# Optimization experiments

Measured on AMD Instinct MI355X. Metric: run time of the kernel, lower is better.

The kernel has to match this reference:

```python
import jax, jax.numpy as jnp
import numpy as np

DIM, HEADS, FEAT = 512, 8, 128
HEAD_DIM = DIM // HEADS
B, N = 1, 2048
EPS = 1e-8


def setup_inputs() -> dict:
    key = jax.random.key(0)
    k1, k2, k3, k4 = jax.random.split(key, 4)
    x = jax.random.normal(k1, (B, N, DIM), dtype=jnp.float32)
    proj_matrix = jax.random.normal(k2, (HEADS, HEAD_DIM, FEAT), dtype=jnp.float32) / np.sqrt(HEAD_DIM)
    W_qkv = jax.random.normal(k3, (DIM, 3 * DIM), dtype=jnp.float32) * np.sqrt(2.0 / DIM)
    W_out = jax.random.normal(k4, (DIM, DIM), dtype=jnp.float32) * np.sqrt(2.0 / DIM)
    b_out = jnp.zeros((DIM,), dtype=jnp.float32)
    return {"x": x, "proj_matrix": proj_matrix, "W_qkv": W_qkv, "W_out": W_out, "b_out": b_out}


def _feature_map(t):
    return jax.nn.elu(t) + 1.0


def reference(x, proj_matrix, W_qkv, W_out, b_out):
    b, n, d = x.shape
    h, hd = HEADS, HEAD_DIM
    qkv = x @ W_qkv                      # (b,n,3d)
    q, k, v = jnp.split(qkv, 3, axis=-1)
    # (b,n,d) -> (b,h,n,hd)
    def to_heads(t):
        return t.reshape(b, n, h, hd).transpose(0, 2, 1, 3)
    q, k, v = to_heads(q), to_heads(k), to_heads(v)
    q_proj = _feature_map(jnp.einsum('bhnd,hdf->bhnf', q, proj_matrix))
    k_proj = _feature_map(jnp.einsum('bhnd,hdf->bhnf', k, proj_matrix))
    # causal linear attention via prefix sums (matches torch cumsum branch)
    k_cum = jnp.cumsum(k_proj, axis=2)                                   # (b,h,n,f)
    kv_cum = jnp.cumsum(k_proj[..., None] * v[..., None, :], axis=2)     # (b,h,n,f,hd)
    attn = jnp.einsum('bhnf,bhnfd->bhnd', q_proj, kv_cum)
    denom = jnp.einsum('bhnf,bhnf->bhn', q_proj, k_cum)[..., None]
    attn = attn / (denom + EPS)
    attn = attn.transpose(0, 2, 1, 3).reshape(b, n, d)
    return attn @ W_out + b_out
```

## Files before the change

### kernel.cpp

```cpp
#include <hip/hip_runtime.h>
#include <math.h>

#define NTOK 2048
#define DMODEL 512
#define NH 8
#define HD 64
#define NF 128
#define QKV_LD 1536
#define CHUNK 64
#define NCHUNK 32
#define EPS_C 1e-8f

typedef __bf16 bf16x8 __attribute__((ext_vector_type(8)));
typedef float f32x4 __attribute__((ext_vector_type(4)));

__device__ inline unsigned short f2bf(float f) {
  union { float f; unsigned u; } v; v.f = f;
  unsigned r = v.u + 0x7FFF + ((v.u >> 16) & 1);
  return (unsigned short)(r >> 16);
}


__global__ __launch_bounds__(256) void pack_all(
    const float* __restrict__ x, const float* __restrict__ W_qkv,
    const float* __restrict__ W_out, const float* __restrict__ proj,
    unsigned short* __restrict__ xpk, unsigned short* __restrict__ wqkvpk,
    unsigned short* __restrict__ woutpk, unsigned short* __restrict__ projpk,
    unsigned short* __restrict__ vT_pk)
{
  const int tid = blockIdx.x * 256 + threadIdx.x;
  const int job = blockIdx.y;
  unsigned short o[8];
  if (job == 0) {
    if (tid >= 131072) return;
    const int lane = tid & 63, blk = tid >> 6;
    const int bk = blk & 15, bm = blk >> 4;
    const int m = bm * 16 + (lane & 15), k = bk * 32 + (lane >> 4) * 8;
    const float4 v0 = *(const float4*)&x[(size_t)m * 512 + k];
    const float4 v1 = *(const float4*)&x[(size_t)m * 512 + k + 4];
    o[0] = f2bf(v0.x); o[1] = f2bf(v0.y); o[2] = f2bf(v0.z); o[3] = f2bf(v0.w);
    o[4] = f2bf(v1.x); o[5] = f2bf(v1.y); o[6] = f2bf(v1.z); o[7] = f2bf(v1.w);
    *(ushort4*)&xpk[(size_t)tid * 8]     = *(ushort4*)&o[0];
    *(ushort4*)&xpk[(size_t)tid * 8 + 4] = *(ushort4*)&o[4];
  } else if (job == 1) {
    if (tid >= 98304) return;
    const int lane = tid & 63, blk = tid >> 6;
    const int bk = blk & 15, bn = blk >> 4;
    const int n = bn * 16 + (lane & 15), k = bk * 32 + (lane >> 4) * 8;
#pragma unroll
    for (int e = 0; e < 8; ++e) o[e] = f2bf(W_qkv[(size_t)(k + e) * QKV_LD + n]);
    *(ushort4*)&wqkvpk[(size_t)tid * 8]     = *(ushort4*)&o[0];
    *(ushort4*)&wqkvpk[(size_t)tid * 8 + 4] = *(ushort4*)&o[4];
  } else if (job == 2) {
    if (tid >= 32768) return;
    const int lane = tid & 63, blk = tid >> 6;
    const int bk = blk & 15, bn = blk >> 4;
    const int n = bn * 16 + (lane & 15), k = bk * 32 + (lane >> 4) * 8;
#pragma unroll
    for (int e = 0; e < 8; ++e) o[e] = f2bf(W_out[(size_t)(k + e) * DMODEL + n]);
    *(ushort4*)&woutpk[(size_t)tid * 8]     = *(ushort4*)&o[0];
    *(ushort4*)&woutpk[(size_t)tid * 8 + 4] = *(ushort4*)&o[4];
  } else if (job == 3) {
    if (tid >= 8192) return;
    const int lane = tid & 63, blk = (tid >> 6) & 15, h = tid >> 10;
    const int bk = blk & 1, bn = blk >> 1;
    const int n = bn * 16 + (lane & 15), k = bk * 32 + (lane >> 4) * 8;
#pragma unroll
    for (int e = 0; e < 8; ++e) o[e] = f2bf(proj[(size_t)h * HD * NF + (size_t)(k + e) * NF + n]);
    *(ushort4*)&projpk[(size_t)tid * 8]     = *(ushort4*)&o[0];
    *(ushort4*)&projpk[(size_t)tid * 8 + 4] = *(ushort4*)&o[4];
  } else {
    if (tid >= 32768) return;
    const int hc = tid >> 7, kt = (tid >> 6) & 1, lane = tid & 63;
    const unsigned short val = ((lane & 15) == 0) ? (unsigned short)0x3F80 : (unsigned short)0;
    const size_t u = (size_t)hc * 640 + (4 * 2 + kt) * 64 + lane;
#pragma unroll
    for (int e = 0; e < 8; ++e) o[e] = val;
    *(ushort4*)&vT_pk[u * 8]     = *(ushort4*)&o[0];
    *(ushort4*)&vT_pk[u * 8 + 4] = *(ushort4*)&o[4];
  }
}

template<bool BIAS, int EMIT>
__global__ __launch_bounds__(256) void gemm_pk(
    const unsigned short* __restrict__ Apk, const unsigned short* __restrict__ Bpk,
    const float* __restrict__ bias, float* __restrict__ Cf,
    unsigned short* __restrict__ qkv_pk, unsigned short* __restrict__ vT_pk,
    int K, int ldc)
{
  const int lane = threadIdx.x & 63, w = threadIdx.x >> 6;
  const int wr = w >> 1, wc = w & 1;
  const int m0 = blockIdx.y * 64 + wr * 32;
  const int n0 = blockIdx.x * 64 + wc * 32;
  const int ks = K >> 5;
  const unsigned short* a0 = Apk + ((size_t)(m0 >> 4) * ks * 64 + lane) * 8;
  const unsigned short* a1 = a0 + (size_t)ks * 512;
  const unsigned short* b0 = Bpk + ((size_t)(n0 >> 4) * ks * 64 + lane) * 8;
  const unsigned short* b1 = b0 + (size_t)ks * 512;
  f32x4 acc00 = {0.f, 0.f, 0.f, 0.f}, acc01 = acc00, acc10 = acc00, acc11 = acc00;
#pragma unroll 4
  for (int s = 0; s < ks; ++s) {
    const bf16x8 af0 = *(const bf16x8*)(a0 + (size_t)s * 512);
    const bf16x8 af1 = *(const bf16x8*)(a1 + (size_t)s * 512);
    const bf16x8 bv0 = *(const bf16x8*)(b0 + (size_t)s * 512);
    const bf16x8 bv1 = *(const bf16x8*)(b1 + (size_t)s * 512);
    acc00 = __builtin_amdgcn_mfma_f32_16x16x32_bf16(af0, bv0, acc00, 0, 0, 0);
    acc01 = __builtin_amdgcn_mfma_f32_16x16x32_bf16(af0, bv1, acc01, 0, 0, 0);
    acc10 = __builtin_amdgcn_mfma_f32_16x16x32_bf16(af1, bv0, acc10, 0, 0, 0);
    acc11 = __builtin_amdgcn_mfma_f32_16x16x32_bf16(af1, bv1, acc11, 0, 0, 0);
  }
  const int r16 = lane & 15, kg = lane >> 4;
#pragma unroll
  for (int mb = 0; mb < 2; ++mb) {
#pragma unroll
    for (int nb = 0; nb < 2; ++nb) {
      const f32x4 a = mb == 0 ? (nb == 0 ? acc00 : acc01) : (nb == 0 ? acc10 : acc11);
      const int col = n0 + nb * 16 + r16;
      if (EMIT == 1) {
        if (col < 1024) {
          const int src = col >> 9, h = (col >> 6) & 7;
          const size_t base = (size_t)(src * 8 + h) * 16384 +
              ((size_t)((m0 >> 4) + mb) * 2 + wc) * 64 +
              ((nb * 2 + (r16 >> 3)) & 3) * 16;
          const int elem = r16 & 7;
#pragma unroll
          for (int r = 0; r < 4; ++r)
            qkv_pk[(base + kg * 4 + r) * 8 + elem] = f2bf(a[r]);
        } else {
          const int h = (col >> 6) - 16, c = blockIdx.y;
          const int vc = col & 63;
          const size_t u = (size_t)(h * 32 + c) * 640 +
              ((size_t)(vc >> 4) * 2 + wr) * 64 + (vc & 15) + (mb * 2 + (kg >> 1)) * 16;
          ushort4 rr;
          rr.x = f2bf(a[0]); rr.y = f2bf(a[1]); rr.z = f2bf(a[2]); rr.w = f2bf(a[3]);
          *(ushort4*)&vT_pk[u * 8 + (kg & 1) * 4] = rr;
        }
      } else {
        const float bv = BIAS ? bias[col] : 0.f;
#pragma unroll
        for (int r = 0; r < 4; ++r)
          Cf[(size_t)(m0 + mb * 16 + kg * 4 + r) * ldc + col] = a[r] + bv;
      }
    }
  }
}

__global__ __launch_bounds__(256) void proj_sums(
    const unsigned short* __restrict__ qkv_pk, const unsigned short* __restrict__ projpk,
    const unsigned short* __restrict__ vT_pk,
    unsigned short* __restrict__ q_pk, unsigned short* __restrict__ k_pk,
    float* __restrict__ kvsum)
{
  __shared__ unsigned short kT[8192];
  const int lane = threadIdx.x & 63, w = threadIdx.x >> 6;
  const int wr = w & 1, wc = w >> 1;
  const int c = blockIdx.x, src = blockIdx.y, h = blockIdx.z;
  const int r16 = lane & 15, kg = lane >> 4;
  const unsigned short* abase = qkv_pk + (size_t)(src * 8 + h) * 16384 * 8;
  const unsigned short* bbase = projpk + (size_t)h * 1024 * 8 + (size_t)lane * 8;
  f32x4 acc[2][4] = {};
#pragma unroll
  for (int s = 0; s < 2; ++s) {
#pragma unroll
    for (int mb = 0; mb < 2; ++mb) {
      const bf16x8 af = *(const bf16x8*)(abase +
          (((size_t)(c * 4 + wr * 2 + mb) * 2 + s) * 64 + lane) * 8);
#pragma unroll
      for (int nb = 0; nb < 4; ++nb) {
        const bf16x8 bv = *(const bf16x8*)(bbase + (size_t)((wc * 4 + nb) * 2 + s) * 512);
        acc[mb][nb] = __builtin_amdgcn_mfma_f32_16x16x32_bf16(af, bv, acc[mb][nb], 0, 0, 0);
      }
    }
  }
  unsigned short* dst = (src ? k_pk : q_pk) + (size_t)h * 32768 * 8;
#pragma unroll
  for (int mb = 0; mb < 2; ++mb) {
#pragma unroll
    for (int nb = 0; nb < 4; ++nb) {
      unsigned short vb[4];
#pragma unroll
      for (int r = 0; r < 4; ++r) {
        const float v = acc[mb][nb][r];
        vb[r] = f2bf(v > 0.f ? v + 1.f : expf(v));
      }
      const size_t base = ((size_t)(c * 4 + wr * 2 + mb) * 4 + wc * 2 + (nb >> 1)) * 64 +
                          ((nb & 1) * 2 + (r16 >> 3)) * 16;
      const int elem = r16 & 7;
#pragma unroll
      for (int r = 0; r < 4; ++r)
        dst[(base + kg * 4 + r) * 8 + elem] = vb[r];
      if (src == 1) {
        const size_t u = ((size_t)(wc * 4 + nb) * 2 + wr) * 64 + r16 + (mb * 2 + (kg >> 1)) * 16;
        *(ushort4*)&kT[u * 8 + (kg & 1) * 4] = *(ushort4*)&vb[0];
      }
    }
  }
  if (src == 1) {
    __syncthreads();
    const int wr2 = w >> 1, wc2 = w & 1;
    const int nnt = wc2 ? 2 : 3;
    const int ntb = wc2 ? 3 : 0;
    const unsigned short* vb_base = vT_pk + (size_t)(h * 32 + c) * 640 * 8;
    f32x4 acc2[4][3] = {};
#pragma unroll
    for (int ks = 0; ks < 2; ++ks) {
      bf16x8 bfr[3];
      for (int j = 0; j < 3; ++j)
        if (j < nnt)
          bfr[j] = *(const bf16x8*)(vb_base + (((size_t)(ntb + j) * 2 + ks) * 64 + lane) * 8);
#pragma unroll
      for (int amb = 0; amb < 4; ++amb) {
        const bf16x8 af = *(const bf16x8*)&kT[((((size_t)(wr2 * 4 + amb)) * 2 + ks) * 64 + lane) * 8];
        for (int j = 0; j < 3; ++j)
          if (j < nnt)
            acc2[amb][j] = __builtin_amdgcn_mfma_f32_16x16x32_bf16(af, bfr[j], acc2[amb][j], 0, 0, 0);
      }
    }
    float* outp = kvsum + (size_t)(h * 32 + c) * 128 * 80;
#pragma unroll
    for (int amb = 0; amb < 4; ++amb)
      for (int j = 0; j < 3; ++j)
        if (j < nnt) {
          const int colv = (ntb + j) * 16 + r16;
#pragma unroll
          for (int r = 0; r < 4; ++r)
            outp[(size_t)(wr2 * 64 + amb * 16 + kg * 4 + r) * 80 + colv] = acc2[amb][j][r];
        }
  }
}

__global__ __launch_bounds__(256) void chunk_scan(
    const float* __restrict__ kvsum, unsigned short* __restrict__ kvpre_pk)
{
  const int tid = blockIdx.x * 256 + threadIdx.x;
  if (tid >= 10240) return;
  const int h = tid / 1280, rem = tid % 1280;
  const int f8 = rem / 80, vc = rem % 80;
  float run[8] = {};
  const size_t u = ((size_t)(vc >> 4) * 4 + (f8 >> 2)) * 64 + (vc & 15) + (f8 & 3) * 16;
  for (int c = 0; c < NCHUNK; ++c) {
    unsigned short o[8];
#pragma unroll
    for (int e = 0; e < 8; ++e) o[e] = f2bf(run[e]);
    unsigned short* dst = kvpre_pk + ((size_t)(h * 32 + c) * 1280 + u) * 8;
    *(ushort4*)&dst[0] = *(ushort4*)&o[0];
    *(ushort4*)&dst[4] = *(ushort4*)&o[4];
    const float* srcp = kvsum + ((size_t)(h * 32 + c) * 128 + f8 * 8) * 80 + vc;
#pragma unroll
    for (int e = 0; e < 8; ++e) run[e] += srcp[(size_t)e * 80];
  }
}

__global__ __launch_bounds__(256) void chunk_attn(
    const unsigned short* __restrict__ q_pk, const unsigned short* __restrict__ k_pk,
    const unsigned short* __restrict__ kvpre_pk, const unsigned short* __restrict__ vT_pk,
    unsigned short* __restrict__ attn_pk)
{
  __shared__ unsigned short P[4096];
  __shared__ float den[64];
  const int lane = threadIdx.x & 63, w = threadIdx.x >> 6;
  const int wr = w >> 1, wc = w & 1;
  const int c = blockIdx.x, h = blockIdx.y;
  const int r16 = lane & 15, kg = lane >> 4;
  const unsigned short* qb = q_pk + (size_t)h * 32768 * 8;
  const unsigned short* kb = k_pk + (size_t)h * 32768 * 8;
  bf16x8 qa[2][4];
#pragma unroll
  for (int amb = 0; amb < 2; ++amb)
#pragma unroll
    for (int ks = 0; ks < 4; ++ks)
      qa[amb][ks] = *(const bf16x8*)(qb +
          (((size_t)(c * 4 + wr * 2 + amb) * 4 + ks) * 64 + lane) * 8);
  {
    f32x4 accS[2][2] = {};
#pragma unroll
    for (int ks = 0; ks < 4; ++ks) {
#pragma unroll
      for (int bnb = 0; bnb < 2; ++bnb) {
        const bf16x8 bf = *(const bf16x8*)(kb +
            (((size_t)(c * 4 + wc * 2 + bnb) * 4 + ks) * 64 + lane) * 8);
#pragma unroll
        for (int amb = 0; amb < 2; ++amb)
          accS[amb][bnb] = __builtin_amdgcn_mfma_f32_16x16x32_bf16(qa[amb][ks], bf, accS[amb][bnb], 0, 0, 0);
      }
    }
#pragma unroll
    for (int amb = 0; amb < 2; ++amb)
#pragma unroll
      for (int bnb = 0; bnb < 2; ++bnb) {
        const int ck = wc * 32 + bnb * 16 + r16;
        const size_t u = ((size_t)(wr * 2 + amb) * 2 + wc) * 64 + (bnb * 2 + (r16 >> 3)) * 16;
        const int elem = r16 & 7;
#pragma unroll
        for (int r = 0; r < 4; ++r) {
          const int rq = wr * 32 + amb * 16 + kg * 4 + r;
          P[(u + kg * 4 + r) * 8 + elem] = (ck <= rq) ? f2bf(accS[amb][bnb][r]) : (unsigned short)0;
        }
      }
  }
  __syncthreads();
  const int nnt = wc ? 2 : 3;
  const int ntb = wc ? 3 : 0;
  const unsigned short* kvp = kvpre_pk + (size_t)(h * 32 + c) * 1280 * 8;
  const unsigned short* vtb = vT_pk + (size_t)(h * 32 + c) * 640 * 8;
  f32x4 acc[2][3] = {};
#pragma unroll
  for (int ks = 0; ks < 4; ++ks) {
    bf16x8 bfr[3];
    for (int j = 0; j < 3; ++j)
      if (j < nnt)
        bfr[j] = *(const bf16x8*)(kvp + (((size_t)(ntb + j) * 4 + ks) * 64 + lane) * 8);
#pragma unroll
    for (int amb = 0; amb < 2; ++amb)
      for (int j = 0; j < 3; ++j)
        if (j < nnt)
          acc[amb][j] = __builtin_amdgcn_mfma_f32_16x16x32_bf16(qa[amb][ks], bfr[j], acc[amb][j], 0, 0, 0);
  }
#pragma unroll
  for (int ks = 0; ks < 2; ++ks) {
    bf16x8 bfr[3];
    for (int j = 0; j < 3; ++j)
      if (j < nnt)
        bfr[j] = *(const bf16x8*)(vtb + (((size_t)(ntb + j) * 2 + ks) * 64 + lane) * 8);
#pragma unroll
    for (int amb = 0; amb < 2; ++amb) {
      const bf16x8 pf = *(const bf16x8*)&P[((((size_t)(wr * 2 + amb)) * 2 + ks) * 64 + lane) * 8];
      for (int j = 0; j < 3; ++j)
        if (j < nnt)
          acc[amb][j] = __builtin_amdgcn_mfma_f32_16x16x32_bf16(pf, bfr[j], acc[amb][j], 0, 0, 0);
    }
  }
  if (wc == 1 && r16 == 0) {
#pragma unroll
    for (int amb = 0; amb < 2; ++amb)
#pragma unroll
      for (int r = 0; r < 4; ++r)
        den[wr * 32 + amb * 16 + kg * 4 + r] = acc[amb][1][r] + EPS_C;
  }
  __syncthreads();
#pragma unroll
  for (int amb = 0; amb < 2; ++amb) {
    for (int j = 0; j < 3; ++j) {
      const int nt = ntb + j;
      if (nt >= 4 || j >= nnt) continue;
      const int acol = h * 64 + nt * 16 + r16;
      const size_t base = ((size_t)(c * 4 + wr * 2 + amb) * 16 + (acol >> 5)) * 64 +
                          ((nt * 2 + (r16 >> 3)) & 3) * 16;
      const int elem = acol & 7;
#pragma unroll
      for (int r = 0; r < 4; ++r) {
        const float dinv = 1.0f / den[wr * 32 + amb * 16 + kg * 4 + r];
        attn_pk[(base + kg * 4 + r) * 8 + elem] = f2bf(acc[amb][j][r] * dinv);
      }
    }
  }
}

extern "C" void kernel_launch(void* const* d_in, const int* in_sizes, int n_in,
                              void* d_out, int out_size, void* d_ws, size_t ws_size,
                              hipStream_t stream) {
  const float* x     = (const float*)d_in[0];
  const float* proj  = (const float*)d_in[1];
  const float* W_qkv = (const float*)d_in[2];
  const float* W_out = (const float*)d_in[3];
  const float* b_out = (const float*)d_in[4];
  float* out = (float*)d_out;

  float* kvsum = (float*)d_ws;
  unsigned short* xpk     = (unsigned short*)(kvsum + 2621440);
  unsigned short* wqkvpk  = xpk + 1048576;
  unsigned short* woutpk  = wqkvpk + 786432;
  unsigned short* projpk  = woutpk + 262144;
  unsigned short* qkv_pk  = projpk + 65536;
  unsigned short* q_pk    = qkv_pk + 2097152;
  unsigned short* k_pk    = q_pk + 2097152;
  unsigned short* vT_pk   = k_pk + 2097152;
  unsigned short* kvpre_pk= vT_pk + 1310720;
  unsigned short* attn_pk = kvpre_pk + 2621440;

  pack_all<<<dim3(512, 5), 256, 0, stream>>>(x, W_qkv, W_out, proj,
                                             xpk, wqkvpk, woutpk, projpk, vT_pk);
  gemm_pk<false, 1><<<dim3(QKV_LD / 64, NTOK / 64), 256, 0, stream>>>(
      xpk, wqkvpk, nullptr, nullptr, qkv_pk, vT_pk, DMODEL, 0);
  proj_sums<<<dim3(NCHUNK, 2, NH), 256, 0, stream>>>(
      qkv_pk, projpk, vT_pk, q_pk, k_pk, kvsum);
  chunk_scan<<<dim3(40), 256, 0, stream>>>(kvsum, kvpre_pk);
  chunk_attn<<<dim3(NCHUNK, NH), 256, 0, stream>>>(
      q_pk, k_pk, kvpre_pk, vT_pk, attn_pk);
  gemm_pk<true, 0><<<dim3(DMODEL / 64, NTOK / 64), 256, 0, stream>>>(
      attn_pk, woutpk, b_out, out, nullptr, nullptr, DMODEL, DMODEL);
}
```

Measured before the change: 55.81 us.

## Fuse QKV GEMM with feature projection and merge chunk sums into scan

The QKV GEMM kernel now stages each 64x64 Q/K tile in shared memory and applies the per-head feature projection and ELU+1 in the same block, writing packed q/k and a transposed k layout directly. The separate proj_sums and chunk_scan kernels are replaced by one sums_scan kernel that computes each chunk's k^T v with MFMA and accumulates the running prefix in registers across chunks. This removes the intermediate qkv_pk and fp32 kvsum round trips and two launches. In exchange the scan is serialized over 32 chunks inside only 40 blocks, which leaves little parallelism in that stage.

```diff
diff --git a/kernel.cpp b/kernel.cpp
--- a/kernel.cpp
+++ b/kernel.cpp
@@ -81,12 +81,142 @@
   }
 }
 
-template<bool BIAS, int EMIT>
-__global__ __launch_bounds__(256) void gemm_pk(
+__global__ __launch_bounds__(256) void qkv_proj(
     const unsigned short* __restrict__ Apk, const unsigned short* __restrict__ Bpk,
-    const float* __restrict__ bias, float* __restrict__ Cf,
-    unsigned short* __restrict__ qkv_pk, unsigned short* __restrict__ vT_pk,
-    int K, int ldc)
+    const unsigned short* __restrict__ projpk,
+    unsigned short* __restrict__ q_pk, unsigned short* __restrict__ k_pk,
+    unsigned short* __restrict__ kT_pk, unsigned short* __restrict__ vT_pk)
+{
+  __shared__ unsigned short QK[4096];
+  const int lane = threadIdx.x & 63, w = threadIdx.x >> 6;
+  const int wr = w >> 1, wc = w & 1;
+  const int c = blockIdx.y;
+  const int m0 = c * 64 + wr * 32;
+  const int n0 = blockIdx.x * 64 + wc * 32;
+  const unsigned short* a0 = Apk + ((size_t)(m0 >> 4) * 16 * 64 + lane) * 8;
+  const unsigned short* a1 = a0 + (size_t)16 * 512;
+  const unsigned short* b0 = Bpk + ((size_t)(n0 >> 4) * 16 * 64 + lane) * 8;
+  const unsigned short* b1 = b0 + (size_t)16 * 512;
+  f32x4 acc00 = {0.f, 0.f, 0.f, 0.f}, acc01 = acc00, acc10 = acc00, acc11 = acc00;
+#pragma unroll 4
+  for (int s = 0; s < 16; ++s) {
+    const bf16x8 af0 = *(const bf16x8*)(a0 + (size_t)s * 512);
+    const bf16x8 af1 = *(const bf16x8*)(a1 + (size_t)s * 512);
+    const bf16x8 bv0 = *(const bf16x8*)(b0 + (size_t)s * 512);
+    const bf16x8 bv1 = *(const bf16x8*)(b1 + (size_t)s * 512);
+    acc00 = __builtin_amdgcn_mfma_f32_16x16x32_bf16(af0, bv0, acc00, 0, 0, 0);
+    acc01 = __builtin_amdgcn_mfma_f32_16x16x32_bf16(af0, bv1, acc01, 0, 0, 0);
+    acc10 = __builtin_amdgcn_mfma_f32_16x16x32_bf16(af1, bv0, acc10, 0, 0, 0);
+    acc11 = __builtin_amdgcn_mfma_f32_16x16x32_bf16(af1, bv1, acc11, 0, 0, 0);
+  }
+  const int r16 = lane & 15, kg = lane >> 4;
+  if (blockIdx.x < 16) {
+    const int src = blockIdx.x >> 3, h = blockIdx.x & 7;
+#pragma unroll
+    for (int mb = 0; mb < 2; ++mb) {
+#pragma unroll
+      for (int nb = 0; nb < 2; ++nb) {
+        const f32x4 a = mb == 0 ? (nb == 0 ? acc00 : acc01) : (nb == 0 ? acc10 : acc11);
+        const size_t u = ((size_t)(wr * 2 + mb) * 2 + wc) * 64 +
+                         (nb * 2 + (r16 >> 3)) * 16 + kg * 4;
+        const int elem = r16 & 7;
+#pragma unroll
+        for (int r = 0; r < 4; ++r)
+          QK[(u + r) * 8 + elem] = f2bf(a[r]);
+      }
+    }
+    __syncthreads();
+    const unsigned short* bbase = projpk + (size_t)h * 8192 + (size_t)lane * 8;
+    f32x4 p[2][4] = {};
+#pragma unroll
+    for (int s = 0; s < 2; ++s) {
+#pragma unroll
+      for (int mb = 0; mb < 2; ++mb) {
+        const bf16x8 af = *(const bf16x8*)&QK[((((size_t)(wr * 2 + mb)) * 2 + s) * 64 + lane) * 8];
+#pragma unroll
+        for (int nb = 0; nb < 4; ++nb) {
+          const bf16x8 bv = *(const bf16x8*)(bbase + (size_t)((wc * 4 + nb) * 2 + s) * 512);
+          p[mb][nb] = __builtin_amdgcn_mfma_f32_16x16x32_bf16(af, bv, p[mb][nb], 0, 0, 0);
+        }
+      }
+    }
+    unsigned short* dst = (src ? k_pk : q_pk) + (size_t)h * 262144;
+#pragma unroll
+    for (int mb = 0; mb < 2; ++mb) {
+#pragma unroll
+      for (int nb = 0; nb < 4; ++nb) {
+        unsigned short vb[4];
+#pragma unroll
+        for (int r = 0; r < 4; ++r) {
+          const float v = p[mb][nb][r];
+          vb[r] = f2bf(v > 0.f ? v + 1.f : expf(v));
+        }
+        const size_t base = ((size_t)(c * 4 + wr * 2 + mb) * 4 + wc * 2 + (nb >> 1)) * 64 +
+                            ((nb & 1) * 2 + (r16 >> 3)) * 16;
+        const int elem = r16 & 7;
+#pragma unroll
+        for (int r = 0; r < 4; ++r)
+          dst[(base + kg * 4 + r) * 8 + elem] = vb[r];
+        if (src == 1) {
+          const size_t u = (size_t)(h * 32 + c) * 1024 +
+              ((size_t)(wc * 4 + nb) * 2 + wr) * 64 + r16 + (mb * 2 + (kg >> 1)) * 16;
+          *(ushort4*)&kT_pk[u * 8 + (kg & 1) * 4] = *(ushort4*)&vb[0];
+        }
+      }
+    }
+  } else {
+    const int h = blockIdx.x - 16;
+#pragma unroll
+    for (int mb = 0; mb < 2; ++mb) {
+#pragma unroll
+      for (int nb = 0; nb < 2; ++nb) {
+        const f32x4 a = mb == 0 ? (nb == 0 ? acc00 : acc01) : (nb == 0 ? acc10 : acc11);
+        const int vc = wc * 32 + nb * 16 + r16;
+        const size_t u = (size_t)(h * 32 + c) * 640 +
+            ((size_t)(vc >> 4) * 2 + wr) * 64 + (vc & 15) + (mb * 2 + (kg >> 1)) * 16;
+        ushort4 rr;
+        rr.x = f2bf(a[0]); rr.y = f2bf(a[1]); rr.z = f2bf(a[2]); rr.w = f2bf(a[3]);
+        *(ushort4*)&vT_pk[u * 8 + (kg & 1) * 4] = rr;
+      }
+    }
+  }
+}
+
+__global__ __launch_bounds__(256) void sums_scan(
+    const unsigned short* __restrict__ kT_pk, const unsigned short* __restrict__ vT_pk,
+    unsigned short* __restrict__ kvpre_pk)
+{
+  const int lane = threadIdx.x & 63, w = threadIdx.x >> 6;
+  const int vt = blockIdx.x, h = blockIdx.y;
+  const int r16 = lane & 15, kg = lane >> 4;
+  f32x4 acc[2] = {};
+  for (int c = 0; c < NCHUNK; ++c) {
+    unsigned short* dst = kvpre_pk + (size_t)(h * 32 + c) * 1280 * 8;
+#pragma unroll
+    for (int mb = 0; mb < 2; ++mb) {
+      unsigned short vb[4];
+#pragma unroll
+      for (int r = 0; r < 4; ++r) vb[r] = f2bf(acc[mb][r]);
+      const size_t u = (size_t)(vt * 4 + w) * 64 + r16 + (mb * 2 + (kg >> 1)) * 16;
+      *(ushort4*)&dst[u * 8 + (kg & 1) * 4] = *(ushort4*)&vb[0];
+    }
+    const unsigned short* kb = kT_pk + (size_t)(h * 32 + c) * 1024 * 8;
+    const unsigned short* vb_ = vT_pk + (size_t)(h * 32 + c) * 640 * 8;
+#pragma unroll
+    for (int s = 0; s < 2; ++s) {
+      const bf16x8 bf = *(const bf16x8*)(vb_ + (((size_t)vt * 2 + s) * 64 + lane) * 8);
+#pragma unroll
+      for (int mb = 0; mb < 2; ++mb) {
+        const bf16x8 af = *(const bf16x8*)(kb + ((((size_t)(w * 2 + mb)) * 2 + s) * 64 + lane) * 8);
+        acc[mb] = __builtin_amdgcn_mfma_f32_16x16x32_bf16(af, bf, acc[mb], 0, 0, 0);
+      }
+    }
+  }
+}
+
+__global__ __launch_bounds__(256) void gemm_out(
+    const unsigned short* __restrict__ Apk, const unsigned short* __restrict__ Bpk,
+    const float* __restrict__ bias, float* __restrict__ Cf, int K, int ldc)
 {
   const int lane = threadIdx.x & 63, w = threadIdx.x >> 6;
   const int wr = w >> 1, wc = w & 1;
@@ -116,138 +246,11 @@
     for (int nb = 0; nb < 2; ++nb) {
       const f32x4 a = mb == 0 ? (nb == 0 ? acc00 : acc01) : (nb == 0 ? acc10 : acc11);
       const int col = n0 + nb * 16 + r16;
-      if (EMIT == 1) {
-        if (col < 1024) {
-          const int src = col >> 9, h = (col >> 6) & 7;
-          const size_t base = (size_t)(src * 8 + h) * 16384 +
-              ((size_t)((m0 >> 4) + mb) * 2 + wc) * 64 +
-              ((nb * 2 + (r16 >> 3)) & 3) * 16;
-          const int elem = r16 & 7;
-#pragma unroll
-          for (int r = 0; r < 4; ++r)
-            qkv_pk[(base + kg * 4 + r) * 8 + elem] = f2bf(a[r]);
-        } else {
-          const int h = (col >> 6) - 16, c = blockIdx.y;
-          const int vc = col & 63;
-          const size_t u = (size_t)(h * 32 + c) * 640 +
-              ((size_t)(vc >> 4) * 2 + wr) * 64 + (vc & 15) + (mb * 2 + (kg >> 1)) * 16;
-          ushort4 rr;
-          rr.x = f2bf(a[0]); rr.y = f2bf(a[1]); rr.z = f2bf(a[2]); rr.w = f2bf(a[3]);
-          *(ushort4*)&vT_pk[u * 8 + (kg & 1) * 4] = rr;
-        }
-      } else {
-        const float bv = BIAS ? bias[col] : 0.f;
-#pragma unroll
-        for (int r = 0; r < 4; ++r)
-          Cf[(size_t)(m0 + mb * 16 + kg * 4 + r) * ldc + col] = a[r] + bv;
-      }
-    }
-  }
-}
-
-__global__ __launch_bounds__(256) void proj_sums(
-    const unsigned short* __restrict__ qkv_pk, const unsigned short* __restrict__ projpk,
-    const unsigned short* __restrict__ vT_pk,
-    unsigned short* __restrict__ q_pk, unsigned short* __restrict__ k_pk,
-    float* __restrict__ kvsum)
-{
-  __shared__ unsigned short kT[8192];
-  const int lane = threadIdx.x & 63, w = threadIdx.x >> 6;
-  const int wr = w & 1, wc = w >> 1;
-  const int c = blockIdx.x, src = blockIdx.y, h = blockIdx.z;
-  const int r16 = lane & 15, kg = lane >> 4;
-  const unsigned short* abase = qkv_pk + (size_t)(src * 8 + h) * 16384 * 8;
-  const unsigned short* bbase = projpk + (size_t)h * 1024 * 8 + (size_t)lane * 8;
-  f32x4 acc[2][4] = {};
-#pragma unroll
-  for (int s = 0; s < 2; ++s) {
-#pragma unroll
-    for (int mb = 0; mb < 2; ++mb) {
-      const bf16x8 af = *(const bf16x8*)(abase +
-          (((size_t)(c * 4 + wr * 2 + mb) * 2 + s) * 64 + lane) * 8);
-#pragma unroll
-      for (int nb = 0; nb < 4; ++nb) {
-        const bf16x8 bv = *(const bf16x8*)(bbase + (size_t)((wc * 4 + nb) * 2 + s) * 512);
-        acc[mb][nb] = __builtin_amdgcn_mfma_f32_16x16x32_bf16(af, bv, acc[mb][nb], 0, 0, 0);
-      }
-    }
-  }
-  unsigned short* dst = (src ? k_pk : q_pk) + (size_t)h * 32768 * 8;
-#pragma unroll
-  for (int mb = 0; mb < 2; ++mb) {
-#pragma unroll
-    for (int nb = 0; nb < 4; ++nb) {
-      unsigned short vb[4];
-#pragma unroll
-      for (int r = 0; r < 4; ++r) {
-        const float v = acc[mb][nb][r];
-        vb[r] = f2bf(v > 0.f ? v + 1.f : expf(v));
-      }
-      const size_t base = ((size_t)(c * 4 + wr * 2 + mb) * 4 + wc * 2 + (nb >> 1)) * 64 +
-                          ((nb & 1) * 2 + (r16 >> 3)) * 16;
-      const int elem = r16 & 7;
+      const float bv = bias[col];
 #pragma unroll
       for (int r = 0; r < 4; ++r)
-        dst[(base + kg * 4 + r) * 8 + elem] = vb[r];
-      if (src == 1) {
-        const size_t u = ((size_t)(wc * 4 + nb) * 2 + wr) * 64 + r16 + (mb * 2 + (kg >> 1)) * 16;
-        *(ushort4*)&kT[u * 8 + (kg & 1) * 4] = *(ushort4*)&vb[0];
-      }
-    }
-  }
-  if (src == 1) {
-    __syncthreads();
-    const int wr2 = w >> 1, wc2 = w & 1;
-    const int nnt = wc2 ? 2 : 3;
-    const int ntb = wc2 ? 3 : 0;
-    const unsigned short* vb_base = vT_pk + (size_t)(h * 32 + c) * 640 * 8;
-    f32x4 acc2[4][3] = {};
-#pragma unroll
-    for (int ks = 0; ks < 2; ++ks) {
-      bf16x8 bfr[3];
-      for (int j = 0; j < 3; ++j)
-        if (j < nnt)
-          bfr[j] = *(const bf16x8*)(vb_base + (((size_t)(ntb + j) * 2 + ks) * 64 + lane) * 8);
-#pragma unroll
-      for (int amb = 0; amb < 4; ++amb) {
-        const bf16x8 af = *(const bf16x8*)&kT[((((size_t)(wr2 * 4 + amb)) * 2 + ks) * 64 + lane) * 8];
-        for (int j = 0; j < 3; ++j)
-          if (j < nnt)
-            acc2[amb][j] = __builtin_amdgcn_mfma_f32_16x16x32_bf16(af, bfr[j], acc2[amb][j], 0, 0, 0);
-      }
-    }
-    float* outp = kvsum + (size_t)(h * 32 + c) * 128 * 80;
-#pragma unroll
-    for (int amb = 0; amb < 4; ++amb)
-      for (int j = 0; j < 3; ++j)
-        if (j < nnt) {
-          const int colv = (ntb + j) * 16 + r16;
-#pragma unroll
-          for (int r = 0; r < 4; ++r)
-            outp[(size_t)(wr2 * 64 + amb * 16 + kg * 4 + r) * 80 + colv] = acc2[amb][j][r];
-        }
-  }
-}
-
-__global__ __launch_bounds__(256) void chunk_scan(
-    const float* __restrict__ kvsum, unsigned short* __restrict__ kvpre_pk)
-{
-  const int tid = blockIdx.x * 256 + threadIdx.x;
-  if (tid >= 10240) return;
-  const int h = tid / 1280, rem = tid % 1280;
-  const int f8 = rem / 80, vc = rem % 80;
-  float run[8] = {};
-  const size_t u = ((size_t)(vc >> 4) * 4 + (f8 >> 2)) * 64 + (vc & 15) + (f8 & 3) * 16;
-  for (int c = 0; c < NCHUNK; ++c) {
-    unsigned short o[8];
-#pragma unroll
-    for (int e = 0; e < 8; ++e) o[e] = f2bf(run[e]);
-    unsigned short* dst = kvpre_pk + ((size_t)(h * 32 + c) * 1280 + u) * 8;
-    *(ushort4*)&dst[0] = *(ushort4*)&o[0];
-    *(ushort4*)&dst[4] = *(ushort4*)&o[4];
-    const float* srcp = kvsum + ((size_t)(h * 32 + c) * 128 + f8 * 8) * 80 + vc;
-#pragma unroll
-    for (int e = 0; e < 8; ++e) run[e] += srcp[(size_t)e * 80];
+        Cf[(size_t)(m0 + mb * 16 + kg * 4 + r) * ldc + col] = a[r] + bv;
+    }
   }
 }
 
@@ -262,8 +265,8 @@
   const int wr = w >> 1, wc = w & 1;
   const int c = blockIdx.x, h = blockIdx.y;
   const int r16 = lane & 15, kg = lane >> 4;
-  const unsigned short* qb = q_pk + (size_t)h * 32768 * 8;
-  const unsigned short* kb = k_pk + (size_t)h * 32768 * 8;
+  const unsigned short* qb = q_pk + (size_t)h * 262144;
+  const unsigned short* kb = k_pk + (size_t)h * 262144;
   bf16x8 qa[2][4];
 #pragma unroll
   for (int amb = 0; amb < 2; ++amb)
@@ -366,27 +369,24 @@
   const float* b_out = (const float*)d_in[4];
   float* out = (float*)d_out;
 
-  float* kvsum = (float*)d_ws;
-  unsigned short* xpk     = (unsigned short*)(kvsum + 2621440);
-  unsigned short* wqkvpk  = xpk + 1048576;
-  unsigned short* woutpk  = wqkvpk + 786432;
-  unsigned short* projpk  = woutpk + 262144;
-  unsigned short* qkv_pk  = projpk + 65536;
-  unsigned short* q_pk    = qkv_pk + 2097152;
-  unsigned short* k_pk    = q_pk + 2097152;
-  unsigned short* vT_pk   = k_pk + 2097152;
-  unsigned short* kvpre_pk= vT_pk + 1310720;
-  unsigned short* attn_pk = kvpre_pk + 2621440;
+  unsigned short* xpk      = (unsigned short*)d_ws;
+  unsigned short* wqkvpk   = xpk + 1048576;
+  unsigned short* woutpk   = wqkvpk + 786432;
+  unsigned short* projpk   = woutpk + 262144;
+  unsigned short* q_pk     = projpk + 65536;
+  unsigned short* k_pk     = q_pk + 2097152;
+  unsigned short* kT_pk    = k_pk + 2097152;
+  unsigned short* vT_pk    = kT_pk + 2097152;
+  unsigned short* kvpre_pk = vT_pk + 1310720;
+  unsigned short* attn_pk  = kvpre_pk + 2621440;
 
   pack_all<<<dim3(512, 5), 256, 0, stream>>>(x, W_qkv, W_out, proj,
                                              xpk, wqkvpk, woutpk, projpk, vT_pk);
-  gemm_pk<false, 1><<<dim3(QKV_LD / 64, NTOK / 64), 256, 0, stream>>>(
-      xpk, wqkvpk, nullptr, nullptr, qkv_pk, vT_pk, DMODEL, 0);
-  proj_sums<<<dim3(NCHUNK, 2, NH), 256, 0, stream>>>(
-      qkv_pk, projpk, vT_pk, q_pk, k_pk, kvsum);
-  chunk_scan<<<dim3(40), 256, 0, stream>>>(kvsum, kvpre_pk);
+  qkv_proj<<<dim3(QKV_LD / 64, NTOK / 64), 256, 0, stream>>>(
+      xpk, wqkvpk, projpk, q_pk, k_pk, kT_pk, vT_pk);
+  sums_scan<<<dim3(5, NH), 256, 0, stream>>>(kT_pk, vT_pk, kvpre_pk);
   chunk_attn<<<dim3(NCHUNK, NH), 256, 0, stream>>>(
       q_pk, k_pk, kvpre_pk, vT_pk, attn_pk);
-  gemm_pk<true, 0><<<dim3(DMODEL / 64, NTOK / 64), 256, 0, stream>>>(
-      attn_pk, woutpk, b_out, out, nullptr, nullptr, DMODEL, DMODEL);
-}
+  gemm_out<<<dim3(DMODEL / 64, NTOK / 64), 256, 0, stream>>>(
+      attn_pk, woutpk, b_out, out, DMODEL, DMODEL);
+}
```

Measured after the change: 52.56 us, median of 2. -5.8%, faster.
